# Optimization experiments

Measured on AMD Instinct MI355X. Metric: run time of the kernel, lower is better.

The kernel has to match this reference:

```python
import jax, jax.numpy as jnp
import numpy as np

IN_SHAPE, OUT_SHAPE = 64, 256  # FoldingBlock(64, 256, ...)
REPEAT = OUT_SHAPE // IN_SHAPE  # 4


def sample_2d(m, n):
    # Reproduces SANet.points + SANet.sample_2D exactly (numpy constants).
    xs = np.linspace(-0.3, 0.3, 46)
    ys = np.linspace(-0.3, 0.3, 46)
    X, Y = np.meshgrid(xs, ys)            # (46,46) each, 'xy' indexing
    pts = np.stack([X, Y])                # (2,46,46)
    ix = np.round(np.linspace(0, 45, m)).astype(int)
    iy = np.round(np.linspace(0, 45, n)).astype(int)
    gx, gy = np.meshgrid(ix, iy)          # (n,m)
    p = pts[:, gx.ravel(), gy.ravel()].T  # (m*n, 2)
    return jnp.asarray(p, dtype=jnp.float32)


def _lin_relu(x, W, b):
    return jax.nn.relu(x @ W + b)


def setup_inputs() -> dict:
    key = jax.random.key(0)
    ks = jax.random.split(key, 16)
    s = 0.02  # small init scale keeps softmax logits well-conditioned
    d = {
        "p": jax.random.normal(ks[0], (128, 64, 512), dtype=jnp.float32),
        # upmlp1: MLP([514, 512]) (shared by both up() calls)
        "W_up": jax.random.normal(ks[1], (514, 512), dtype=jnp.float32) * s,
        "b_up": jnp.zeros((512,), jnp.float32),
        # self_attn1: M_h = MLP([1024,256])
        "Wh": jax.random.normal(ks[2], (1024, 256), dtype=jnp.float32) * s,
        "bh": jnp.zeros((256,), jnp.float32),
        # M_l = MLP([1024,256])
        "Wl": jax.random.normal(ks[3], (1024, 256), dtype=jnp.float32) * s,
        "bl": jnp.zeros((256,), jnp.float32),
        # M_g = MLP([1024,1024])
        "Wg": jax.random.normal(ks[4], (1024, 1024), dtype=jnp.float32) * s,
        "bg": jnp.zeros((1024,), jnp.float32),
        # M_f = MLP([1024,512,256]) -> two Linear+ReLU layers
        "Wf1": jax.random.normal(ks[5], (1024, 512), dtype=jnp.float32) * s,
        "bf1": jnp.zeros((512,), jnp.float32),
        "Wf2": jax.random.normal(ks[6], (512, 256), dtype=jnp.float32) * s,
        "bf2": jnp.zeros((256,), jnp.float32),
        # M_down: MLP([1024, 512])
        "W_down": jax.random.normal(ks[7], (1024, 512), dtype=jnp.float32) * s,
        "b_down": jnp.zeros((512,), jnp.float32),
        "m": 16,
        "n": 16,
    }
    return d


def _up(p, pts, W_up, b_up, Wh, bh, Wl, bl, Wg, bg, Wf1, bf1, Wf2, bf2):
    # p: (B, 64, 512) -> (B, 256, 512) via torch-style repeat (tile)
    B = p.shape[0]
    p = jnp.tile(p, (1, REPEAT, 1))
    p2d = jnp.concatenate([p, jnp.broadcast_to(pts[None], (B,) + pts.shape)], -1)  # (B,256,514)
    p2d = _lin_relu(p2d, W_up, b_up)                  # (B,256,512)
    p = jnp.concatenate([p, p2d], -1)                  # (B,256,1024)
    # SelfAttention (hand-rolled: separate projections + softmax + bmm)
    h = _lin_relu(p, Wh, bh)                           # (B,256,256)
    l = _lin_relu(p, Wl, bl)                           # (B,256,256)
    g = _lin_relu(p, Wg, bg)                           # (B,256,1024)
    mm = jnp.einsum("bmc,bnc->bmn", l, h)             # l @ h^T
    attn = jax.nn.softmax(mm, axis=-1)
    applied = jnp.einsum("bmn,bnc->bmc", attn, g)      # (B,256,1024)
    x = p + applied
    # M_f = MLP([1024,512,256]): ReLU after every Linear
    return _lin_relu(_lin_relu(x, Wf1, bf1), Wf2, bf2)  # (B,256,256)


def _down(p, W_down, b_down):
    # (B,256,256) -> (B,64,1024) -> MLP([1024,512])
    B = p.shape[0]
    p = p.reshape(B, IN_SHAPE, REPEAT * p.shape[2])
    return _lin_relu(p, W_down, b_down)                # (B,64,512)


def reference(p, W_up, b_up, Wh, bh, Wl, bl, Wg, bg, Wf1, bf1, Wf2, bf2,
              W_down, b_down, m, n):
    pts = sample_2d(int(m), int(n))                    # (m*n, 2) constant grid
    attn_params = (Wh, bh, Wl, bl, Wg, bg, Wf1, bf1, Wf2, bf2)
    p1 = _up(p, pts, W_up, b_up, *attn_params)         # (B,256,256)
    p2 = _down(p1, W_down, b_down)                     # (B,64,512)
    p_delta = p - p2
    p2u = _up(p_delta, pts, W_up, b_up, *attn_params)  # shared weights with first up
    return p1 + p2u                                    # (B,256,256)
```

## Files before the change

kernel.cpp:

```cpp
#include <hip/hip_runtime.h>
#include <cstdint>
#include <cstddef>


typedef unsigned short u16;
typedef __bf16 bf16x8 __attribute__((ext_vector_type(8)));
typedef float f32x4 __attribute__((ext_vector_type(4)));

__device__ __forceinline__ u16 f2bf(float f) {
    unsigned u = __builtin_bit_cast(unsigned, f);
    unsigned r = (u + 0x7fffu + ((u >> 16) & 1u)) >> 16;
    return (u16)r;
}
__device__ __forceinline__ float bf2f(u16 h) {
    unsigned u = ((unsigned)h) << 16;
    return __builtin_bit_cast(float, u);
}
__device__ __forceinline__ bf16x8 ldfrag(const u16* p) {
    return __builtin_bit_cast(bf16x8, *reinterpret_cast<const uint4*>(p));
}
__device__ __forceinline__ void gload16(const u16* g, u16* l) {
    __builtin_amdgcn_global_load_lds((__attribute__((address_space(1))) void*)g,
                                     (__attribute__((address_space(3))) void*)l,
                                     16, 0, 0);
}
__device__ __forceinline__ unsigned ldsaddr(const u16* p) {
    return (unsigned)(size_t)(const __attribute__((address_space(3))) u16*)p;
}
__device__ __forceinline__ bf16x8 dsr128(unsigned a) {
    f32x4 r;
    asm volatile("ds_read_b128 %0, %1" : "=v"(r) : "v"(a));
    return __builtin_bit_cast(bf16x8, r);
}

#define FENCE asm volatile("" ::: "memory")
#define BAR() do { FENCE; __builtin_amdgcn_s_barrier(); FENCE; } while (0)
#define VMC(N) asm volatile("s_waitcnt vmcnt(" #N ")" ::: "memory")
#define LGKM(N) do { asm volatile("s_waitcnt lgkmcnt(" #N ")" ::: "memory"); \
                     __builtin_amdgcn_sched_barrier(0); } while (0)

__device__ __forceinline__ int xcd_swz(int lin, int nwg) {
    if ((nwg & 7) == 0) { const int q = nwg >> 3; lin = (lin & 7) * q + (lin >> 3); }
    return lin;
}

template<int MODE>
__global__ __launch_bounds__(512, 1)
void bp(const u16* __restrict__ A0, const u16* __restrict__ A1,
        const u16* __restrict__ Bt, const float* __restrict__ bias,
        const float* __restrict__ EXf, const u16* __restrict__ EXb,
        u16* __restrict__ outB, u16* __restrict__ out1, u16* __restrict__ out2,
        int K, long sB)
{
    __shared__ __align__(16) u16 As[2][16384];
    __shared__ __align__(16) u16 Bs[2][16384];

    const int lin = xcd_swz(blockIdx.y * gridDim.x + blockIdx.x,
                            gridDim.x * gridDim.y);
    const int b    = lin / gridDim.x;
    const int gn0  = (lin % gridDim.x) * 256;
    const int tid  = threadIdx.x;
    const int lane = tid & 63;
    const int w    = tid >> 6;
    const int wr   = w >> 2, wc = w & 3;
    const int wrow0 = wr * 128, wcol0 = wc * 64;
    const int lm   = lane & 15, hk = lane >> 4;
    const int NT   = K / 64;

    const int srow = tid & 255;
    const int su   = tid >> 8;

    const u16* gA0;
    const u16* gA1 = nullptr;
    if constexpr (MODE == 1) {
        gA0 = A0 + ((size_t)b << 15) + (size_t)(srow & 63) * 512 + su * 8;
        gA1 = A1 + ((size_t)b << 17) + (size_t)srow * 512 + su * 8;
    } else if constexpr (MODE == 3) {
        gA0 = A0 + ((size_t)b << 16) + (size_t)srow * 256 + su * 8;
    } else {
        gA0 = A0 + ((size_t)b << 18) + (size_t)srow * 1024 + su * 8;
    }
    const u16* gB0 = Bt + (size_t)b * sB + (size_t)(gn0 + srow) * K + su * 8;

    u16* dA = &As[0][(size_t)(su * 256 + srow) * 8];
    u16* dB = &Bs[0][(size_t)(su * 256 + srow) * 8];

    auto stgA = [&](int kt, int buf, int rp) {
        const u16* g;
        if constexpr (MODE == 1) g = (kt < 8) ? (gA0 + kt * 64) : (gA1 + (kt - 8) * 64);
        else                     g = gA0 + kt * 64;
        u16* d = dA + buf * 16384 + rp * 8192;
        gload16(g + rp * 32,      d);
        gload16(g + rp * 32 + 16, d + 4096);
    };
    auto stgB = [&](int kt, int buf, int rp) {
        const u16* g = gB0 + kt * 64 + rp * 32;
        u16* d = dB + buf * 16384 + rp * 8192;
        gload16(g,      d);
        gload16(g + 16, d + 4096);
    };

    const u16* rA = &As[0][(size_t)(hk * 256 + wrow0 + lm) * 8];
    const u16* rB = &Bs[0][(size_t)(hk * 256 + wcol0 + lm) * 8];

    f32x4 acc[8][4];
    #pragma unroll
    for (int i = 0; i < 8; ++i)
        #pragma unroll
        for (int j = 0; j < 4; ++j)
            acc[i][j] = (f32x4){0.f, 0.f, 0.f, 0.f};

    stgA(0, 0, 0); stgA(0, 0, 1);
    stgB(0, 0, 0); stgB(0, 0, 1);
    stgA(1, 1, 0); stgB(1, 1, 0);
    VMC(4);
    BAR();

    for (int t = 0; t < NT; ++t) {
        const int buf = t & 1, nx = buf ^ 1;
        const u16* a  = rA + buf * 16384;
        const u16* bb = rB + buf * 16384;
        bf16x8 aq[4], bq[4];
        const bool dupA = (MODE == 1) && (t < 8);

        #pragma unroll
        for (int i = 0; i < 4; ++i) aq[i] = ldfrag(a + i * 128);
        #pragma unroll
        for (int j = 0; j < 4; ++j) bq[j] = ldfrag(bb + j * 128);
        if (t + 1 < NT) stgA(t + 1, nx, 1);
        BAR();
        __builtin_amdgcn_s_setprio(1);
        #pragma unroll
        for (int i = 0; i < 4; ++i)
            #pragma unroll
            for (int j = 0; j < 4; ++j)
                acc[i][j] = __builtin_amdgcn_mfma_f32_16x16x32_bf16(aq[i], bq[j], acc[i][j], 0, 0, 0);
        __builtin_amdgcn_s_setprio(0);
        BAR();

        if (!dupA) {
            #pragma unroll
            for (int i = 0; i < 4; ++i) aq[i] = ldfrag(a + (4 + i) * 128);
        }
        if (t + 1 < NT) stgB(t + 1, nx, 1);
        BAR();
        __builtin_amdgcn_s_setprio(1);
        #pragma unroll
        for (int i = 0; i < 4; ++i)
            #pragma unroll
            for (int j = 0; j < 4; ++j)
                acc[4 + i][j] = __builtin_amdgcn_mfma_f32_16x16x32_bf16(aq[i], bq[j], acc[4 + i][j], 0, 0, 0);
        __builtin_amdgcn_s_setprio(0);
        BAR();

        #pragma unroll
        for (int i = 0; i < 4; ++i) aq[i] = ldfrag(a + 8192 + i * 128);
        #pragma unroll
        for (int j = 0; j < 4; ++j) bq[j] = ldfrag(bb + 8192 + j * 128);
        if (t + 2 < NT) stgA(t + 2, buf, 0);
        BAR();
        __builtin_amdgcn_s_setprio(1);
        #pragma unroll
        for (int i = 0; i < 4; ++i)
            #pragma unroll
            for (int j = 0; j < 4; ++j)
                acc[i][j] = __builtin_amdgcn_mfma_f32_16x16x32_bf16(aq[i], bq[j], acc[i][j], 0, 0, 0);
        __builtin_amdgcn_s_setprio(0);
        BAR();

        if (!dupA) {
            #pragma unroll
            for (int i = 0; i < 4; ++i) aq[i] = ldfrag(a + 8192 + (4 + i) * 128);
        }
        if (t + 2 < NT) stgB(t + 2, buf, 0);
        if (t + 2 < NT) { VMC(4); } else { VMC(0); }
        BAR();
        __builtin_amdgcn_s_setprio(1);
        #pragma unroll
        for (int i = 0; i < 4; ++i)
            #pragma unroll
            for (int j = 0; j < 4; ++j)
                acc[4 + i][j] = __builtin_amdgcn_mfma_f32_16x16x32_bf16(aq[i], bq[j], acc[4 + i][j], 0, 0, 0);
        __builtin_amdgcn_s_setprio(0);
        BAR();
    }

    #pragma unroll
    for (int i = 0; i < 8; ++i) {
        const int rowb = wrow0 + i * 16 + hk * 4;
        #pragma unroll
        for (int j = 0; j < 4; ++j) {
            const int col = gn0 + wcol0 + j * 16 + lm;
            float v4[4];
            #pragma unroll
            for (int r = 0; r < 4; ++r) v4[r] = acc[i][j][r];

            if constexpr (MODE == 1) {
                if (col < 512) {
                    #pragma unroll
                    for (int r = 0; r < 4; ++r) {
                        const int row = rowb + r;
                        float v = fmaxf(v4[r] + bias[col], 0.0f);
                        if (col < 256) outB[((size_t)b << 16) + (size_t)row * 256 + col] = f2bf(v);
                        else           out1[((size_t)b << 16) + (size_t)row * 256 + (col - 256)] = f2bf(v);
                    }
                } else {
                    ushort4 o;
                    o.x = f2bf(fmaxf(v4[0] + bias[col], 0.0f));
                    o.y = f2bf(fmaxf(v4[1] + bias[col], 0.0f));
                    o.z = f2bf(fmaxf(v4[2] + bias[col], 0.0f));
                    o.w = f2bf(fmaxf(v4[3] + bias[col], 0.0f));
                    *reinterpret_cast<ushort4*>(out2 + ((size_t)b << 18) +
                        (size_t)(col - 512) * 256 + rowb) = o;
                }
            } else if constexpr (MODE == 3) {
                #pragma unroll
                for (int r = 0; r < 4; ++r) {
                    const int row = rowb + r;
                    float v = v4[r];
                    float cv;
                    if (col < 512) {
                        const size_t ridx = ((size_t)b << 15) + (size_t)(row & 63) * 512 + col;
                        cv = EXf ? EXf[ridx] : bf2f(EXb[ridx]);
                    } else {
                        cv = bf2f(A1[((size_t)b << 17) + (size_t)row * 512 + (col - 512)]);
                    }
                    v += cv;
                    outB[((size_t)b << 18) + (size_t)row * 1024 + col] = f2bf(v);
                }
            } else {
                #pragma unroll
                for (int r = 0; r < 4; ++r) {
                    const int row = rowb + r;
                    float v = fmaxf(v4[r] + bias[col], 0.0f);
                    outB[((size_t)b << 17) + (size_t)row * 512 + col] = f2bf(v);
                }
            }
        }
    }
}

__global__ __launch_bounds__(512, 4)
void sp(const u16* __restrict__ A0, const u16* __restrict__ Bt,
        const float* __restrict__ bias, const float* __restrict__ EXf,
        u16* __restrict__ outB, int K)
{
    __shared__ __align__(16) u16 As[2][4096];
    __shared__ __align__(16) u16 Bs[2][8192];

    const int bz   = blockIdx.z;
    const int gn0  = blockIdx.x * 256;
    const int tid  = threadIdx.x;
    const int lane = tid & 63;
    const int w    = tid >> 6;
    const int wr   = w >> 2, wc = w & 3;
    const int wrow0 = wr * 64, wcol0 = wc * 64;
    const int lm   = lane & 15, hk = lane >> 4;
    const int NT   = K / 32;

    const int rowA = tid & 127, uA = tid >> 7;
    const int rowB = tid & 255, uB = tid >> 8;

    const u16* gA = A0 + ((size_t)(2 * bz + (rowA >> 6)) << 15)
                       + (size_t)(rowA & 63) * 512 + uA * 8;
    const u16* gB0 = Bt + (size_t)(gn0 + rowB) * K + uB * 8;
    const u16* gB1 = gB0 + 16;

    u16* dA  = &As[0][(size_t)(uA * 128 + rowA) * 8];
    u16* dB0 = &Bs[0][(size_t)(uB * 256 + rowB) * 8];
    u16* dB1 = dB0 + 4096;

    auto stage = [&](int kt, int buf) {
        const int ko = kt * 32;
        gload16(gA  + ko, dA  + buf * 4096);
        gload16(gB0 + ko, dB0 + buf * 8192);
        gload16(gB1 + ko, dB1 + buf * 8192);
    };

    const unsigned aB = ldsaddr(&As[0][0]) + (unsigned)((hk * 128 + wrow0 + lm) * 16);
    const unsigned bB = ldsaddr(&Bs[0][0]) + (unsigned)((hk * 256 + wcol0 + lm) * 16);

    f32x4 acc[4][4];
    #pragma unroll
    for (int i = 0; i < 4; ++i)
        #pragma unroll
        for (int j = 0; j < 4; ++j)
            acc[i][j] = (f32x4){0.f, 0.f, 0.f, 0.f};

    stage(0, 0);
    stage(1, 1);

    for (int t = 0; t < NT; ++t) {
        const int buf = t & 1;
        if (t == NT - 1) { VMC(0); } else { VMC(3); }
        BAR();
        bf16x8 aq[4], bq[4];
        const unsigned ab = aB + (unsigned)buf * 8192u;
        const unsigned bb = bB + (unsigned)buf * 16384u;
        #pragma unroll
        for (int i = 0; i < 4; ++i) aq[i] = dsr128(ab + (unsigned)(i * 256));
        #pragma unroll
        for (int j = 0; j < 4; ++j) bq[j] = dsr128(bb + (unsigned)(j * 256));
        LGKM(0);
        __builtin_amdgcn_s_setprio(1);
        #pragma unroll
        for (int i = 0; i < 4; ++i)
            #pragma unroll
            for (int j = 0; j < 4; ++j)
                acc[i][j] = __builtin_amdgcn_mfma_f32_16x16x32_bf16(aq[i], bq[j], acc[i][j], 0, 0, 0);
        __builtin_amdgcn_s_setprio(0);
        BAR();
        if (t + 2 < NT) stage(t + 2, buf);
    }

    #pragma unroll
    for (int i = 0; i < 4; ++i) {
        const int lrb = wrow0 + i * 16 + hk * 4;
        const int b2  = 2 * bz + (lrb >> 6);
        #pragma unroll
        for (int j = 0; j < 4; ++j) {
            const int col = gn0 + wcol0 + j * 16 + lm;
            const float wx = EXf[(size_t)512 * 512 + col];
            const float wy = EXf[(size_t)513 * 512 + col];
            const float bc = bias[col];
            #pragma unroll
            for (int r = 0; r < 4; ++r) {
                const int prow = (lrb + r) & 63;
                const float py = -0.3f + 0.04f * (float)(prow & 15);
                const float base = acc[i][j][r] + py * wy + bc;
                #pragma unroll
                for (int q = 0; q < 4; ++q) {
                    const float px = -0.3f + 0.04f * (float)((prow >> 4) + 4 * q);
                    const float v = fmaxf(base + px * wx, 0.0f);
                    outB[((size_t)b2 << 17) + (size_t)(prow + 64 * q) * 512 + col] = f2bf(v);
                }
            }
        }
    }
}

__global__ __launch_bounds__(256, 1)
void msm(const u16* __restrict__ L, const u16* __restrict__ H,
         u16* __restrict__ attn)
{
    __shared__ __align__(16) u16 As[2][8192];
    __shared__ __align__(16) u16 Bs[2][16384];
    __shared__ float smax[2][2][64];
    __shared__ float ssum[2][2][64];

    const int b    = blockIdx.z;
    const int gm0  = blockIdx.y * 128;
    const int tid  = threadIdx.x;
    const int lane = tid & 63;
    const int w    = tid >> 6;
    const int wr   = w >> 1, wc = w & 1;
    const int lm   = lane & 15, hk = lane >> 4;

    auto stage = [&](int kt, int buf) {
        const int kb = kt * 64;
        #pragma unroll
        for (int t = 0; t < 4; ++t) {
            const int idx = tid + t * 256;
            const int U = idx >> 7, row = idx & 127;
            gload16(L + ((size_t)b << 16) + (size_t)(gm0 + row) * 256 + kb + U * 8,
                    &As[buf][(size_t)idx * 8]);
        }
        #pragma unroll
        for (int t = 0; t < 8; ++t) {
            const int idx = tid + t * 256;
            const int U = idx >> 8, row = idx & 255;
            gload16(H + ((size_t)b << 16) + (size_t)row * 256 + kb + U * 8,
                    &Bs[buf][(size_t)idx * 8]);
        }
    };

    f32x4 acc[4][8];
    #pragma unroll
    for (int i = 0; i < 4; ++i)
        #pragma unroll
        for (int j = 0; j < 8; ++j)
            acc[i][j] = (f32x4){0.f, 0.f, 0.f, 0.f};

    stage(0, 0);
    stage(1, 1);

    for (int kt = 0; kt < 4; ++kt) {
        const int cur = kt & 1;
        if (kt == 3) { VMC(0); } else { VMC(12); }
        BAR();
        #pragma unroll
        for (int ks = 0; ks < 2; ++ks) {
            bf16x8 aq[4], bq[8];
            #pragma unroll
            for (int i = 0; i < 4; ++i)
                aq[i] = ldfrag(&As[cur][(size_t)((ks * 4 + hk) * 128 + wr * 64 + i * 16 + lm) * 8]);
            #pragma unroll
            for (int j = 0; j < 8; ++j)
                bq[j] = ldfrag(&Bs[cur][(size_t)((ks * 4 + hk) * 256 + wc * 128 + j * 16 + lm) * 8]);
            #pragma unroll
            for (int i = 0; i < 4; ++i)
                #pragma unroll
                for (int j = 0; j < 8; ++j)
                    acc[i][j] = __builtin_amdgcn_mfma_f32_16x16x32_bf16(aq[i], bq[j], acc[i][j], 0, 0, 0);
        }
        BAR();
        if (kt + 2 < 4) stage(kt + 2, cur);
    }

    float m[4][4];
    #pragma unroll
    for (int i = 0; i < 4; ++i)
        #pragma unroll
        for (int r = 0; r < 4; ++r) {
            float mm = acc[i][0][r];
            #pragma unroll
            for (int j = 1; j < 8; ++j) mm = fmaxf(mm, acc[i][j][r]);
            #pragma unroll
            for (int o = 1; o < 16; o <<= 1) mm = fmaxf(mm, __shfl_xor(mm, o));
            m[i][r] = mm;
        }
    if (lm == 0) {
        #pragma unroll
        for (int i = 0; i < 4; ++i)
            #pragma unroll
            for (int r = 0; r < 4; ++r)
                smax[wr][wc][i * 16 + hk * 4 + r] = m[i][r];
    }
    __syncthreads();
    #pragma unroll
    for (int i = 0; i < 4; ++i)
        #pragma unroll
        for (int r = 0; r < 4; ++r) {
            const int lr = i * 16 + hk * 4 + r;
            m[i][r] = fmaxf(smax[wr][0][lr], smax[wr][1][lr]);
        }
    float sv[4][4];
    #pragma unroll
    for (int i = 0; i < 4; ++i)
        #pragma unroll
        for (int r = 0; r < 4; ++r) {
            float s = 0.f;
            #pragma unroll
            for (int j = 0; j < 8; ++j) {
                const float e = expf(acc[i][j][r] - m[i][r]);
                acc[i][j][r] = e;
                s += e;
            }
            #pragma unroll
            for (int o = 1; o < 16; o <<= 1) s += __shfl_xor(s, o);
            sv[i][r] = s;
        }
    if (lm == 0) {
        #pragma unroll
        for (int i = 0; i < 4; ++i)
            #pragma unroll
            for (int r = 0; r < 4; ++r)
                ssum[wr][wc][i * 16 + hk * 4 + r] = sv[i][r];
    }
    __syncthreads();
    #pragma unroll
    for (int i = 0; i < 4; ++i) {
        #pragma unroll
        for (int r = 0; r < 4; ++r) {
            const int lr = i * 16 + hk * 4 + r;
            const float inv = 1.0f / (ssum[wr][0][lr] + ssum[wr][1][lr]);
            const int row = gm0 + wr * 64 + lr;
            #pragma unroll
            for (int j = 0; j < 8; ++j) {
                const int col = wc * 128 + j * 16 + lm;
                attn[((size_t)b << 16) + (size_t)row * 256 + col] = f2bf(acc[i][j][r] * inv);
            }
        }
    }
}

template<int MODE>
__global__ __launch_bounds__(256, 2)
void mg(const u16* __restrict__ A0, const u16* __restrict__ Bt,
        const float* __restrict__ bias, const float* __restrict__ EXf,
        float* __restrict__ outF, u16* __restrict__ outB,
        int K, long sB)
{
    constexpr int BK = 64;
    constexpr int UMASK = 7;

    __shared__ __align__(16) u16 As[2][128 * 64];
    __shared__ __align__(16) u16 Bs[2][128 * 64];

    const int b    = blockIdx.z;
    const int tid  = threadIdx.x;
    const int lane = tid & 63;
    const int w    = tid >> 6;
    const int wr   = w >> 1, wc = w & 1;
    const int wrow0 = wr * 64, wcol0 = wc * 64;
    const int gm0  = blockIdx.y * 128;
    const int gn0  = blockIdx.x * 128;
    const int lm   = lane & 15, hk = lane >> 4;
    const int NT = K / BK;

    auto stage = [&](int kt, int buf) {
        const int kb = kt * BK;
        #pragma unroll
        for (int t = 0; t < 4; ++t) {
            const int idx = tid + t * 256;
            const int row = idx >> 3, u = idx & UMASK;
            const int kk = kb + ((u ^ (row & UMASK)) << 3);
            const u16* ga;
            if constexpr (MODE == 5) {
                ga = A0 + ((size_t)b << 17) + (size_t)(gm0 + row) * 512 + kk;
            } else {
                int gr = gm0 + row; if (gr > 63) gr = 63;
                ga = A0 + ((size_t)b << 16) + (size_t)(gr * 4 + (kk >> 8)) * 256 + (kk & 255);
            }
            gload16(ga, &As[buf][(size_t)(w * 64 + t * 256) * 8]);
        }
        #pragma unroll
        for (int t = 0; t < 4; ++t) {
            const int idx = tid + t * 256;
            const int row = idx >> 3, u = idx & UMASK;
            const int kk = kb + ((u ^ (row & UMASK)) << 3);
            gload16(Bt + (size_t)b * sB + (size_t)(gn0 + row) * K + kk,
                    &Bs[buf][(size_t)(w * 64 + t * 256) * 8]);
        }
    };

    f32x4 acc[4][4];
    #pragma unroll
    for (int i = 0; i < 4; ++i)
        #pragma unroll
        for (int j = 0; j < 4; ++j)
            acc[i][j] = (f32x4){0.f, 0.f, 0.f, 0.f};

    stage(0, 0);
    if (NT > 1) stage(1, 1);

    for (int kt = 0; kt < NT; ++kt) {
        const int cur = kt & 1;
        if (kt == NT - 1) { VMC(0); } else { VMC(8); }
        __builtin_amdgcn_s_barrier();
        FENCE;

        #pragma unroll
        for (int ks = 0; ks < 2; ++ks) {
            bf16x8 af[4], bfr[4];
            #pragma unroll
            for (int i = 0; i < 4; ++i) {
                const int row = wrow0 + i * 16 + lm;
                af[i] = ldfrag(&As[cur][(size_t)row * BK + (((ks * 4 + hk) ^ (row & UMASK)) << 3)]);
            }
            #pragma unroll
            for (int j = 0; j < 4; ++j) {
                const int row = wcol0 + j * 16 + lm;
                bfr[j] = ldfrag(&Bs[cur][(size_t)row * BK + (((ks * 4 + hk) ^ (row & UMASK)) << 3)]);
            }
            __builtin_amdgcn_s_setprio(1);
            #pragma unroll
            for (int i = 0; i < 4; ++i)
                #pragma unroll
                for (int j = 0; j < 4; ++j)
                    acc[i][j] = __builtin_amdgcn_mfma_f32_16x16x32_bf16(af[i], bfr[j], acc[i][j], 0, 0, 0);
            __builtin_amdgcn_s_setprio(0);
        }

        FENCE;
        __builtin_amdgcn_s_barrier();
        if (kt + 2 < NT) stage(kt + 2, cur);
    }

    #pragma unroll
    for (int i = 0; i < 4; ++i) {
        #pragma unroll
        for (int r = 0; r < 4; ++r) {
            const int row = gm0 + wrow0 + i * 16 + hk * 4 + r;
            if (MODE == 6 && row >= 64) continue;
            #pragma unroll
            for (int j = 0; j < 4; ++j) {
                const int col = gn0 + wcol0 + j * 16 + lm;
                float v = acc[i][j][r];
                if constexpr (MODE == 5) {
                    v = fmaxf(v + bias[col], 0.0f);
                    const size_t oidx = ((size_t)b << 16) + (size_t)row * 256 + col;
                    if (EXf) v += EXf[oidx];
                    outF[oidx] = v;
                    if (outB) outB[oidx] = f2bf(v);
                } else {
                    v = fmaxf(v + bias[col], 0.0f);
                    const size_t oidx = ((size_t)b << 15) + (size_t)row * 512 + col;
                    v = EXf[oidx] - v;
                    outB[oidx] = f2bf(v);
                }
            }
        }
    }
}

template<bool F32IN>
__global__ __launch_bounds__(256)
void transpose_k(const void* __restrict__ in_, u16* __restrict__ out, int R, int C)
{
    __shared__ float t[64][65];
    const size_t zo = (size_t)blockIdx.z * (size_t)R * C;
    const int c0 = blockIdx.x * 64, r0 = blockIdx.y * 64;
    const int x = threadIdx.x, y = threadIdx.y;
    #pragma unroll
    for (int i = 0; i < 16; ++i) {
        const int r = y * 16 + i;
        float v;
        if constexpr (F32IN) v = ((const float*)in_)[zo + (size_t)(r0 + r) * C + c0 + x];
        else                 v = bf2f(((const u16*)in_)[zo + (size_t)(r0 + r) * C + c0 + x]);
        t[r][x] = v;
    }
    __syncthreads();
    #pragma unroll
    for (int i = 0; i < 16; ++i) {
        const int c = y * 16 + i;
        out[zo + (size_t)(c0 + c) * R + r0 + x] = f2bf(t[x][c]);
    }
}

__global__ __launch_bounds__(256)
void cvt_k(const float* __restrict__ in, u16* __restrict__ out, int n4)
{
    int i = blockIdx.x * 256 + threadIdx.x;
    const int stride = gridDim.x * 256;
    for (; i < n4; i += stride) {
        float4 v = ((const float4*)in)[i];
        ushort4 o;
        o.x = f2bf(v.x); o.y = f2bf(v.y); o.z = f2bf(v.z); o.w = f2bf(v.w);
        ((ushort4*)out)[i] = o;
    }
}

__global__ __launch_bounds__(512)
void concat3_k(const float* __restrict__ a, const float* __restrict__ bb,
               const float* __restrict__ c, float* __restrict__ o)
{
    const int i = blockIdx.x * 512 + threadIdx.x;
    if (i < 256)       o[i] = a[i];
    else if (i < 512)  o[i] = bb[i - 256];
    else if (i < 1536) o[i] = c[i - 512];
}

extern "C" void kernel_launch(void* const* d_in, const int* in_sizes, int n_in,
                              void* d_out, int out_size, void* d_ws, size_t ws_size,
                              hipStream_t stream)
{
    const float* p      = (const float*)d_in[0];
    const float* W_up   = (const float*)d_in[1];
    const float* b_up   = (const float*)d_in[2];
    const float* Wh     = (const float*)d_in[3];
    const float* bh     = (const float*)d_in[4];
    const float* Wl     = (const float*)d_in[5];
    const float* bl     = (const float*)d_in[6];
    const float* Wg     = (const float*)d_in[7];
    const float* bg_    = (const float*)d_in[8];
    const float* Wf1    = (const float*)d_in[9];
    const float* bf1    = (const float*)d_in[10];
    const float* Wf2    = (const float*)d_in[11];
    const float* bf2v   = (const float*)d_in[12];
    const float* W_down = (const float*)d_in[13];
    const float* b_down = (const float*)d_in[14];

    const int B = in_sizes[0] / 32768;
    float* out = (float*)d_out;

    char* wsp = (char*)d_ws;
    auto alloc = [&](size_t bytes) -> char* {
        char* r = wsp; wsp += (bytes + 255) & ~(size_t)255; return r;
    };

    u16* WupT  = (u16*)alloc((size_t)512 * 512 * 2);
    u16* WhlgT = (u16*)alloc((size_t)1536 * 1024 * 2);
    u16* Wf1T  = (u16*)alloc((size_t)512 * 1024 * 2);
    u16* Wf2T  = (u16*)alloc((size_t)256 * 512 * 2);
    u16* WdT   = (u16*)alloc((size_t)512 * 1024 * 2);
    float* bias_hlg = (float*)alloc((size_t)1536 * 4);
    u16* pbf   = (u16*)alloc((size_t)B * 32768 * 2);

    const size_t fixed_used = (size_t)(wsp - (char*)d_ws);
    const size_t perB = 1903104;
    int BC = B;
    while (BC > 1 && fixed_used + (size_t)BC * perB + 4096 > ws_size) BC >>= 1;

    u16* upout = (u16*)alloc((size_t)BC * 131072 * 2);
    u16* gT    = (u16*)alloc((size_t)BC * 262144 * 2);
    u16* xb    = (u16*)alloc((size_t)BC * 262144 * 2);
    u16* hb    = (u16*)alloc((size_t)BC * 65536 * 2);
    u16* lb    = (u16*)alloc((size_t)BC * 65536 * 2);
    u16* atb   = (u16*)alloc((size_t)BC * 65536 * 2);
    u16* p1bf  = (u16*)alloc((size_t)BC * 65536 * 2);
    u16* pdbf  = (u16*)alloc((size_t)BC * 32768 * 2);

    const dim3 tb(64, 4);
    {
        int n4 = B * 8192;
        int nb = (n4 + 255) / 256; if (nb > 2048) nb = 2048;
        cvt_k<<<dim3(nb), dim3(256), 0, stream>>>(p, pbf, n4);
        transpose_k<true><<<dim3(8, 8, 1),  tb, 0, stream>>>(W_up, WupT, 512, 512);
        transpose_k<true><<<dim3(4, 16, 1), tb, 0, stream>>>(Wh, WhlgT, 1024, 256);
        transpose_k<true><<<dim3(4, 16, 1), tb, 0, stream>>>(Wl, WhlgT + (size_t)256 * 1024, 1024, 256);
        transpose_k<true><<<dim3(16, 16, 1),tb, 0, stream>>>(Wg, WhlgT + (size_t)512 * 1024, 1024, 1024);
        transpose_k<true><<<dim3(8, 16, 1), tb, 0, stream>>>(Wf1, Wf1T, 1024, 512);
        transpose_k<true><<<dim3(4, 8, 1),  tb, 0, stream>>>(Wf2, Wf2T, 512, 256);
        transpose_k<true><<<dim3(8, 16, 1), tb, 0, stream>>>(W_down, WdT, 1024, 512);
        concat3_k<<<dim3(3), dim3(512), 0, stream>>>(bh, bl, bg_, bias_hlg);
    }

    auto run_up = [&](const u16* pin_bf, const float* pin_f32, const u16* pin_ebf,
                      float* f2outF, u16* f2outB, const float* f2EXf, int bc) {
        sp<<<dim3(2, 1, bc / 2), dim3(512), 0, stream>>>(
            pin_bf, WupT, b_up, W_up, upout, 512);
        bp<1><<<dim3(6, bc), dim3(512), 0, stream>>>(
            pin_bf, upout, WhlgT, bias_hlg, nullptr, nullptr, hb, lb, gT, 1024, 0);
        msm<<<dim3(1, 2, bc), dim3(256), 0, stream>>>(lb, hb, atb);
        bp<3><<<dim3(4, bc), dim3(512), 0, stream>>>(
            atb, upout, gT, nullptr, pin_f32, pin_ebf, xb, nullptr, nullptr, 256, 262144);
        bp<4><<<dim3(2, bc), dim3(512), 0, stream>>>(
            xb, nullptr, Wf1T, bf1, nullptr, nullptr, upout, nullptr, nullptr, 1024, 0);
        mg<5><<<dim3(2, 2, bc), dim3(256), 0, stream>>>(
            upout, Wf2T, bf2v, f2EXf, f2outF, f2outB, 512, 0);
    };

    for (int b0 = 0; b0 < B; b0 += BC) {
        const int bc = (B - b0 < BC) ? (B - b0) : BC;
        const u16*   pin_bf  = pbf + (size_t)b0 * 32768;
        const float* pin_f32 = p   + (size_t)b0 * 32768;
        float* outc = out + (size_t)b0 * 65536;
        run_up(pin_bf, pin_f32, nullptr, outc, p1bf, nullptr, bc);
        mg<6><<<dim3(4, 1, bc), dim3(256), 0, stream>>>(
            p1bf, WdT, b_down, pin_f32, nullptr, pdbf, 1024, 0);
        run_up(pdbf, nullptr, pdbf, outc, nullptr, outc, bc);
    }
}
```

Measured before the change: 833.3 us.

## Merge GEMM main-loop phases from four barrier-separated stages into two

Restructures the inner K loop of the MFMA GEMM so each half-tile loads all eight A fragments and four B fragments up front, then issues all 32 MFMAs in one prioritized block. This halves the number of block barriers and setprio toggles per iteration, and stgA/stgB global-to-LDS prefetches are issued together. The cost is higher register pressure from holding eight A fragments, which may reduce occupancy. It also gives less interleaving of loads with compute.

```diff
diff --git a/kernel.cpp b/kernel.cpp
--- a/kernel.cpp
+++ b/kernel.cpp
@@ -120,14 +120,18 @@
         const int buf = t & 1, nx = buf ^ 1;
         const u16* a  = rA + buf * 16384;
         const u16* bb = rB + buf * 16384;
-        bf16x8 aq[4], bq[4];
+        bf16x8 aq[8], bq[4];
         const bool dupA = (MODE == 1) && (t < 8);
 
         #pragma unroll
         for (int i = 0; i < 4; ++i) aq[i] = ldfrag(a + i * 128);
+        if (!dupA) {
+            #pragma unroll
+            for (int i = 0; i < 4; ++i) aq[4 + i] = ldfrag(a + (4 + i) * 128);
+        }
         #pragma unroll
         for (int j = 0; j < 4; ++j) bq[j] = ldfrag(bb + j * 128);
-        if (t + 1 < NT) stgA(t + 1, nx, 1);
+        if (t + 1 < NT) { stgA(t + 1, nx, 1); stgB(t + 1, nx, 1); }
         BAR();
         __builtin_amdgcn_s_setprio(1);
         #pragma unroll
@@ -135,44 +139,25 @@
             #pragma unroll
             for (int j = 0; j < 4; ++j)
                 acc[i][j] = __builtin_amdgcn_mfma_f32_16x16x32_bf16(aq[i], bq[j], acc[i][j], 0, 0, 0);
+        #pragma unroll
+        for (int i = 0; i < 4; ++i) {
+            const bf16x8 av = dupA ? aq[i] : aq[4 + i];
+            #pragma unroll
+            for (int j = 0; j < 4; ++j)
+                acc[4 + i][j] = __builtin_amdgcn_mfma_f32_16x16x32_bf16(av, bq[j], acc[4 + i][j], 0, 0, 0);
+        }
         __builtin_amdgcn_s_setprio(0);
         BAR();
 
+        #pragma unroll
+        for (int i = 0; i < 4; ++i) aq[i] = ldfrag(a + 8192 + i * 128);
         if (!dupA) {
             #pragma unroll
-            for (int i = 0; i < 4; ++i) aq[i] = ldfrag(a + (4 + i) * 128);
-        }
-        if (t + 1 < NT) stgB(t + 1, nx, 1);
-        BAR();
-        __builtin_amdgcn_s_setprio(1);
-        #pragma unroll
-        for (int i = 0; i < 4; ++i)
-            #pragma unroll
-            for (int j = 0; j < 4; ++j)
-                acc[4 + i][j] = __builtin_amdgcn_mfma_f32_16x16x32_bf16(aq[i], bq[j], acc[4 + i][j], 0, 0, 0);
-        __builtin_amdgcn_s_setprio(0);
-        BAR();
-
-        #pragma unroll
-        for (int i = 0; i < 4; ++i) aq[i] = ldfrag(a + 8192 + i * 128);
+            for (int i = 0; i < 4; ++i) aq[4 + i] = ldfrag(a + 8192 + (4 + i) * 128);
+        }
         #pragma unroll
         for (int j = 0; j < 4; ++j) bq[j] = ldfrag(bb + 8192 + j * 128);
-        if (t + 2 < NT) stgA(t + 2, buf, 0);
-        BAR();
-        __builtin_amdgcn_s_setprio(1);
-        #pragma unroll
-        for (int i = 0; i < 4; ++i)
-            #pragma unroll
-            for (int j = 0; j < 4; ++j)
-                acc[i][j] = __builtin_amdgcn_mfma_f32_16x16x32_bf16(aq[i], bq[j], acc[i][j], 0, 0, 0);
-        __builtin_amdgcn_s_setprio(0);
-        BAR();
-
-        if (!dupA) {
-            #pragma unroll
-            for (int i = 0; i < 4; ++i) aq[i] = ldfrag(a + 8192 + (4 + i) * 128);
-        }
-        if (t + 2 < NT) stgB(t + 2, buf, 0);
+        if (t + 2 < NT) { stgA(t + 2, buf, 0); stgB(t + 2, buf, 0); }
         if (t + 2 < NT) { VMC(4); } else { VMC(0); }
         BAR();
         __builtin_amdgcn_s_setprio(1);
@@ -180,7 +165,14 @@
         for (int i = 0; i < 4; ++i)
             #pragma unroll
             for (int j = 0; j < 4; ++j)
-                acc[4 + i][j] = __builtin_amdgcn_mfma_f32_16x16x32_bf16(aq[i], bq[j], acc[4 + i][j], 0, 0, 0);
+                acc[i][j] = __builtin_amdgcn_mfma_f32_16x16x32_bf16(aq[i], bq[j], acc[i][j], 0, 0, 0);
+        #pragma unroll
+        for (int i = 0; i < 4; ++i) {
+            const bf16x8 av = dupA ? aq[i] : aq[4 + i];
+            #pragma unroll
+            for (int j = 0; j < 4; ++j)
+                acc[4 + i][j] = __builtin_amdgcn_mfma_f32_16x16x32_bf16(av, bq[j], acc[4 + i][j], 0, 0, 0);
+        }
         __builtin_amdgcn_s_setprio(0);
         BAR();
     }
```

Result: slower. 865.0 us (+3.8%).
